# Optimization experiments

Measured on AMD Instinct MI355X. Metric: run time of the kernel, lower is better.

Reference implementation:

```python
import jax, jax.numpy as jnp
import numpy as np

B, N, M, K = 1, 200000, 100000, 16
C_IN, C_OUT, GFL, HEADS = 64, 128, 32, 8
C4 = C_OUT // 4          # 32, unary1 bottleneck width
C_MID = 16               # weightnet output channels


def _lin(key, fan_in, fan_out):
    return jax.random.normal(key, (fan_in, fan_out), jnp.float32) / np.sqrt(fan_in)


def setup_inputs() -> dict:
    key = jax.random.key(0)
    ks = jax.random.split(key, 20)
    return {
        'dense_xyz': jax.random.normal(ks[0], (B, N, 3), jnp.float32),
        'dense_feats': jax.random.normal(ks[1], (B, N, C_IN), jnp.float32),
        'dense_xyz_norm': jax.random.normal(ks[2], (B, N, 3), jnp.float32),
        'sparse_xyz': jax.random.normal(ks[3], (B, M, 3), jnp.float32),
        'sparse_xyz_norm': jax.random.normal(ks[4], (B, M, 3), jnp.float32),
        'vi_features': jax.random.normal(ks[5], (B, M, K, 12), jnp.float32),
        'nei_inds': jax.random.randint(ks[6], (B, M, K), 0, N),
        # unary1: in -> out/4 (Linear + BN(eval,init) + LeakyReLU(0.1))
        'w_unary1': _lin(ks[7], C_IN, C4), 'b_unary1': jnp.zeros((C4,), jnp.float32),
        # guidance_unary: out/4 -> GFL, no relu
        'w_gu': _lin(ks[8], C4, GFL), 'b_gu': jnp.zeros((GFL,), jnp.float32),
        # mlp_conv: 12 -> GFL (positional encoding on VI features)
        'w_pe': _lin(ks[9], 12, GFL), 'b_pe': jnp.zeros((GFL,), jnp.float32),
        # MultiHeadGuidance (subtraction): 2*GFL -> 8 -> HEADS
        'w_g1': _lin(ks[10], 2 * GFL, 8), 'b_g1': jnp.zeros((8,), jnp.float32),
        'w_g2': _lin(ks[11], 8, HEADS), 'b_g2': jnp.zeros((HEADS,), jnp.float32),
        # WeightNet: 12 -> 8 -> 8 -> 16, relu after each
        'w_wn1': _lin(ks[12], 12, 8), 'b_wn1': jnp.zeros((8,), jnp.float32),
        'w_wn2': _lin(ks[13], 8, 8), 'b_wn2': jnp.zeros((8,), jnp.float32),
        'w_wn3': _lin(ks[14], 8, C_MID), 'b_wn3': jnp.zeros((C_MID,), jnp.float32),
        # linear: out/4 * C_MID -> out/2
        'w_lin': _lin(ks[15], C4 * C_MID, C_OUT // 2), 'b_lin': jnp.zeros((C_OUT // 2,), jnp.float32),
        # unary2: out/2 -> out, no relu
        'w_u2': _lin(ks[16], C_OUT // 2, C_OUT), 'b_u2': jnp.zeros((C_OUT,), jnp.float32),
        # unary_shortcut: in -> out, no relu
        'w_sc': _lin(ks[17], C_IN, C_OUT), 'b_sc': jnp.zeros((C_OUT,), jnp.float32),
    }


def _gather(points, idx):
    # points: [B, N, C], idx: [B, M, K] int -> [B, M, K, C]
    return jax.vmap(lambda p, i: p[i])(points, idx)


def reference(dense_xyz, dense_feats, dense_xyz_norm, sparse_xyz, sparse_xyz_norm,
              vi_features, nei_inds,
              w_unary1, b_unary1, w_gu, b_gu, w_pe, b_pe,
              w_g1, b_g1, w_g2, b_g2,
              w_wn1, b_wn1, w_wn2, b_wn2, w_wn3, b_wn3,
              w_lin, b_lin, w_u2, b_u2, w_sc, b_sc):
    b, m, k = nei_inds.shape
    # unary1 (Linear+BN@init folds to Linear, LeakyReLU 0.1)
    feats_x = jax.nn.leaky_relu(dense_feats @ w_unary1 + b_unary1, 0.1)  # [B,N,C4]
    # USE_VI=True with precomputed vi_features -> weightNetInput = vi_features
    weightnet_input = vi_features                                        # [B,M,K,12]
    feat_pe = jax.nn.relu(weightnet_input @ w_pe + b_pe)                 # [B,M,K,GFL]
    guidance_x = feats_x @ w_gu + b_gu                                   # [B,N,GFL] (no_relu)
    gathered_g = _gather(guidance_x, nei_inds)                           # [B,M,K,GFL]
    g_feat = jnp.concatenate([gathered_g, feat_pe], axis=-1)             # [B,M,K,2*GFL]
    # subtraction guidance: query - max-pooled key over neighborhood
    scores = g_feat - jnp.max(g_feat, axis=2, keepdims=True)
    scores = jax.nn.relu(scores @ w_g1 + b_g1)
    scores = jax.nn.sigmoid(scores @ w_g2 + b_g2)                        # [B,M,K,H]
    gathered_feat = _gather(feats_x, nei_inds)                           # [B,M,K,C4]
    nf = gathered_feat.reshape(b, m, k, HEADS, C4 // HEADS) * scores[..., None]
    nf = nf.reshape(b, m, k, C4)
    # WeightNet on VI features
    w = jax.nn.relu(weightnet_input @ w_wn1 + b_wn1)
    w = jax.nn.relu(w @ w_wn2 + b_wn2)
    w = jax.nn.relu(w @ w_wn3 + b_wn3)                                   # [B,M,K,C_MID]
    # weighted neighbor aggregation: feat^T @ weights per point
    agg = jnp.einsum('bmkc,bmkw->bmcw', nf, w).reshape(b, m, C4 * C_MID)
    out = jax.nn.relu(agg @ w_lin + b_lin)                               # [B,M,out/2]
    out = out @ w_u2 + b_u2                                              # unary2, no relu
    # strided shortcut: max-pool dense feats over neighborhood, then unary
    sparse_feats = jnp.max(_gather(dense_feats, nei_inds), axis=2)       # [B,M,C_IN]
    shortcut = sparse_feats @ w_sc + b_sc
    return jax.nn.leaky_relu(out + shortcut, 0.1)                        # [B,M,C_OUT]
```

## Files before the change

### kernel.cpp

```cpp
#include <hip/hip_runtime.h>
#include <math.h>

typedef __attribute__((ext_vector_type(8))) __bf16 bf16x8;
typedef __attribute__((ext_vector_type(4))) __bf16 bf16x4;
typedef __attribute__((ext_vector_type(4))) float f32x4;

__device__ __forceinline__ float rowmax16(float x) {
    int xi = __builtin_bit_cast(int, x);
    float y;
    y = __builtin_bit_cast(float, __builtin_amdgcn_update_dpp(0, xi, 0x128, 0xf, 0xf, true));
    x = fmaxf(x, y); xi = __builtin_bit_cast(int, x);
    y = __builtin_bit_cast(float, __builtin_amdgcn_update_dpp(0, xi, 0x124, 0xf, 0xf, true));
    x = fmaxf(x, y); xi = __builtin_bit_cast(int, x);
    y = __builtin_bit_cast(float, __builtin_amdgcn_update_dpp(0, xi, 0x122, 0xf, 0xf, true));
    x = fmaxf(x, y); xi = __builtin_bit_cast(int, x);
    y = __builtin_bit_cast(float, __builtin_amdgcn_update_dpp(0, xi, 0x121, 0xf, 0xf, true));
    x = fmaxf(x, y);
    return x;
}

__global__ void prep_kernel(const float* __restrict__ wlin,
                            const float* __restrict__ wu2,
                            const float* __restrict__ wsc,
                            const float* __restrict__ w1,
                            const float* __restrict__ wg,
                            __bf16* __restrict__ wlinT,
                            __bf16* __restrict__ wu2T,
                            __bf16* __restrict__ wscT,
                            __bf16* __restrict__ w1Th,
                            __bf16* __restrict__ w1Tl,
                            __bf16* __restrict__ wgT)
{
    const int B0 = 64 * 512;
    const int B1 = B0 + 128 * 64;
    const int B2 = B1 + 128 * 64;
    const int B3 = B2 + 32 * 64;
    const int B4 = B3 + 32 * 32;
    int i = blockIdx.x * 256 + threadIdx.x;
    if (i < B0) {
        int l = i >> 9, k = i & 511;
        wlinT[i] = (__bf16)wlin[k * 64 + l];
    } else if (i < B1) {
        int j = i - B0; int co = j >> 6, kk = j & 63;
        wu2T[j] = (__bf16)wu2[kk * 128 + co];
    } else if (i < B2) {
        int j = i - B1; int co = j >> 6, kk = j & 63;
        wscT[j] = (__bf16)wsc[kk * 128 + co];
    } else if (i < B3) {
        int j = i - B2; int c = j >> 6, k = j & 63;
        float v = w1[k * 32 + c];
        __bf16 h = (__bf16)v;
        w1Th[j] = h;
        w1Tl[j] = (__bf16)(v - (float)h);
    } else if (i < B4) {
        int j = i - B3; int c = j >> 5, k = j & 31;
        wgT[j] = (__bf16)wg[k * 32 + c];
    }
}

__global__ __launch_bounds__(256) void feats_kernel(
    const float* __restrict__ df,
    const __bf16* __restrict__ w1Th, const __bf16* __restrict__ w1Tl,
    const float* __restrict__ b1,
    const __bf16* __restrict__ wgT, const float* __restrict__ bg,
    __bf16* __restrict__ fxb, __bf16* __restrict__ gxb,
    __bf16* __restrict__ dfb, int N)
{
    __shared__ __bf16 sFx[4][16][40];
    int t = threadIdx.x;
    int wv = t >> 6, ln = t & 63;
    int row = ln & 15, quad = ln >> 4;
    long n0 = (long)blockIdx.x * 64 + wv * 16;
    long n = n0 + row;
    bool ok = n < (long)N;

    const float4* dp = (const float4*)(df + (ok ? n * 64 : 0));
    float4 f00 = dp[quad * 2 + 0], f01 = dp[quad * 2 + 1];
    float4 f10 = dp[8 + quad * 2 + 0], f11 = dp[8 + quad * 2 + 1];
    float s0[8] = {f00.x, f00.y, f00.z, f00.w, f01.x, f01.y, f01.z, f01.w};
    float s1[8] = {f10.x, f10.y, f10.z, f10.w, f11.x, f11.y, f11.z, f11.w};
    bf16x8 aH0, aL0, aH1, aL1;
#pragma unroll
    for (int e = 0; e < 8; e++) {
        __bf16 h = (__bf16)s0[e]; aH0[e] = h; aL0[e] = (__bf16)(s0[e] - (float)h);
        __bf16 g = (__bf16)s1[e]; aH1[e] = g; aL1[e] = (__bf16)(s1[e] - (float)g);
    }
    if (ok) {
        *(bf16x8*)(dfb + n * 64 + quad * 8) = aH0;
        *(bf16x8*)(dfb + n * 64 + 32 + quad * 8) = aH1;
    }

    const __bf16* bh = w1Th + (row * 64 + quad * 8);
    const __bf16* bl = w1Tl + (row * 64 + quad * 8);
    f32x4 acc0 = {0.f, 0.f, 0.f, 0.f}, acc1 = {0.f, 0.f, 0.f, 0.f};
    {
        bf16x8 bH00 = *(const bf16x8*)(bh);
        bf16x8 bH01 = *(const bf16x8*)(bh + 32);
        bf16x8 bH10 = *(const bf16x8*)(bh + 16 * 64);
        bf16x8 bH11 = *(const bf16x8*)(bh + 16 * 64 + 32);
        bf16x8 bL00 = *(const bf16x8*)(bl);
        bf16x8 bL01 = *(const bf16x8*)(bl + 32);
        bf16x8 bL10 = *(const bf16x8*)(bl + 16 * 64);
        bf16x8 bL11 = *(const bf16x8*)(bl + 16 * 64 + 32);
        acc0 = __builtin_amdgcn_mfma_f32_16x16x32_bf16(aH0, bH00, acc0, 0, 0, 0);
        acc0 = __builtin_amdgcn_mfma_f32_16x16x32_bf16(aH1, bH01, acc0, 0, 0, 0);
        acc0 = __builtin_amdgcn_mfma_f32_16x16x32_bf16(aL0, bH00, acc0, 0, 0, 0);
        acc0 = __builtin_amdgcn_mfma_f32_16x16x32_bf16(aL1, bH01, acc0, 0, 0, 0);
        acc0 = __builtin_amdgcn_mfma_f32_16x16x32_bf16(aH0, bL00, acc0, 0, 0, 0);
        acc0 = __builtin_amdgcn_mfma_f32_16x16x32_bf16(aH1, bL01, acc0, 0, 0, 0);
        acc1 = __builtin_amdgcn_mfma_f32_16x16x32_bf16(aH0, bH10, acc1, 0, 0, 0);
        acc1 = __builtin_amdgcn_mfma_f32_16x16x32_bf16(aH1, bH11, acc1, 0, 0, 0);
        acc1 = __builtin_amdgcn_mfma_f32_16x16x32_bf16(aL0, bH10, acc1, 0, 0, 0);
        acc1 = __builtin_amdgcn_mfma_f32_16x16x32_bf16(aL1, bH11, acc1, 0, 0, 0);
        acc1 = __builtin_amdgcn_mfma_f32_16x16x32_bf16(aH0, bL10, acc1, 0, 0, 0);
        acc1 = __builtin_amdgcn_mfma_f32_16x16x32_bf16(aH1, bL11, acc1, 0, 0, 0);
    }
    {
        float bb0 = b1[row], bb1 = b1[16 + row];
#pragma unroll
        for (int r = 0; r < 4; r++) {
            float x0 = acc0[r] + bb0; x0 = x0 > 0.f ? x0 : 0.1f * x0;
            float x1 = acc1[r] + bb1; x1 = x1 > 0.f ? x1 : 0.1f * x1;
            sFx[wv][quad * 4 + r][row] = (__bf16)x0;
            sFx[wv][quad * 4 + r][16 + row] = (__bf16)x1;
        }
    }
    __builtin_amdgcn_s_waitcnt(0);

    f32x4 g0 = {0.f, 0.f, 0.f, 0.f}, g1 = {0.f, 0.f, 0.f, 0.f};
    {
        bf16x8 a2 = *(const bf16x8*)(&sFx[wv][row][quad * 8]);
        bf16x8 b20 = *(const bf16x8*)(wgT + row * 32 + quad * 8);
        bf16x8 b21 = *(const bf16x8*)(wgT + (16 + row) * 32 + quad * 8);
        g0 = __builtin_amdgcn_mfma_f32_16x16x32_bf16(a2, b20, g0, 0, 0, 0);
        g1 = __builtin_amdgcn_mfma_f32_16x16x32_bf16(a2, b21, g1, 0, 0, 0);
    }
    {
        int r16 = ln >> 2, seg = ln & 3;
        bf16x8 vfx = *(const bf16x8*)(&sFx[wv][r16][seg * 8]);
        long nn = n0 + r16;
        if (nn < (long)N) *(bf16x8*)(fxb + nn * 32 + seg * 8) = vfx;
    }
    {
        float bb0 = bg[row], bb1 = bg[16 + row];
#pragma unroll
        for (int r = 0; r < 4; r++) {
            sFx[wv][quad * 4 + r][row] = (__bf16)(g0[r] + bb0);
            sFx[wv][quad * 4 + r][16 + row] = (__bf16)(g1[r] + bb1);
        }
    }
    __builtin_amdgcn_s_waitcnt(0);
    {
        int r16 = ln >> 2, seg = ln & 3;
        bf16x8 vg = *(const bf16x8*)(&sFx[wv][r16][seg * 8]);
        long nn = n0 + r16;
        if (nn < (long)N) *(bf16x8*)(gxb + nn * 32 + seg * 8) = vg;
    }
}

struct SmemU {
    union {
        struct { __bf16 nfF[16 * 512]; __bf16 w3A[16 * 256]; } a;
        __bf16 aggB[16][520];
    };
};

__global__ __launch_bounds__(256, 5) void pcf_kernel(
    const float* __restrict__ vi, const int* __restrict__ nei,
    const __bf16* __restrict__ fxb, const __bf16* __restrict__ gxb,
    const __bf16* __restrict__ dfb,
    const float* __restrict__ wpe, const float* __restrict__ bpe,
    const float* __restrict__ wg1, const float* __restrict__ bg1,
    const float* __restrict__ wg2, const float* __restrict__ bg2,
    const float* __restrict__ wn1, const float* __restrict__ bn1,
    const float* __restrict__ wn2, const float* __restrict__ bn2,
    const float* __restrict__ wn3, const float* __restrict__ bn3,
    const __bf16* __restrict__ wlinT, const float* __restrict__ blin,
    const __bf16* __restrict__ wu2T, const float* __restrict__ bu2,
    const __bf16* __restrict__ wscT, const float* __restrict__ bsc,
    float* __restrict__ out, int M)
{
    __shared__ SmemU U;
    __shared__ __bf16 sO[16][72];
    __shared__ __bf16 sS[16][72];
    __shared__ int sInd[16][16];

    int t = threadIdx.x;
    int p = t >> 4, q = t & 15;
    long mbase = (long)blockIdx.x * 16;
    long m = mbase + p;
    bool okm = m < (long)M;
    int ind = okm ? nei[m * 16 + q] : 0;
    sInd[p][q] = ind;

    float v[12];
    {
        const float4* v4 = (const float4*)(vi + (okm ? (m * 16 + q) * 12 : 0));
        float4 a = v4[0], b = v4[1], cc = v4[2];
        v[0] = a.x; v[1] = a.y; v[2] = a.z; v[3] = a.w;
        v[4] = b.x; v[5] = b.y; v[6] = b.z; v[7] = b.w;
        v[8] = cc.x; v[9] = cc.y; v[10] = cc.z; v[11] = cc.w;
    }
    {
        float wa[8], wb[8];
#pragma unroll
        for (int j = 0; j < 8; j++) {
            float a = bn1[j];
#pragma unroll
            for (int i = 0; i < 12; i++) a += v[i] * wn1[i * 8 + j];
            wa[j] = fmaxf(a, 0.f);
        }
#pragma unroll
        for (int j = 0; j < 8; j++) {
            float a = bn2[j];
#pragma unroll
            for (int i = 0; i < 8; i++) a += wa[i] * wn2[i * 8 + j];
            wb[j] = fmaxf(a, 0.f);
        }
        int swz = (p & 3) << 4;
        int kb = (q >> 3) * 128 + (q & 7);
#pragma unroll
        for (int j = 0; j < 16; j++) {
            float a = bn3[j];
#pragma unroll
            for (int i = 0; i < 8; i++) a += wb[i] * wn3[i * 16 + j];
            U.a.w3A[p * 256 + ((kb + j * 8) ^ swz)] = (__bf16)fmaxf(a, 0.f);
        }
    }
    float pe[32];
#pragma unroll
    for (int c = 0; c < 32; c++) {
        float a = bpe[c];
#pragma unroll
        for (int i = 0; i < 12; i++) a += v[i] * wpe[i * 32 + c];
        pe[c] = fmaxf(a, 0.f);
    }
    float gd[32];
    {
        const bf16x8* g8 = (const bf16x8*)(gxb + (long)ind * 32);
#pragma unroll
        for (int c8 = 0; c8 < 4; c8++) {
            bf16x8 g = g8[c8];
#pragma unroll
            for (int e = 0; e < 8; e++) gd[c8 * 8 + e] = (float)g[e];
        }
    }
    float s1[8];
#pragma unroll
    for (int j = 0; j < 8; j++) s1[j] = bg1[j];
#pragma unroll
    for (int i = 0; i < 64; i++) {
        float gi = (i < 32) ? gd[i] : pe[i - 32];
        float sub = gi - rowmax16(gi);
#pragma unroll
        for (int j = 0; j < 8; j++) s1[j] += sub * wg1[i * 8 + j];
    }
#pragma unroll
    for (int j = 0; j < 8; j++) s1[j] = fmaxf(s1[j], 0.f);
    float s2[8];
#pragma unroll
    for (int j = 0; j < 8; j++) {
        float a = bg2[j];
#pragma unroll
        for (int i = 0; i < 8; i++) a += s1[i] * wg2[i * 8 + j];
        s2[j] = 1.f / (1.f + __expf(-a));
    }
    {
        const bf16x8* f8 = (const bf16x8*)(fxb + (long)ind * 32);
        int swz = (p & 3) << 4;
#pragma unroll
        for (int g = 0; g < 4; g++) {
            bf16x8 f = f8[g];
            float sA = s2[2 * g], sB = s2[2 * g + 1];
#pragma unroll
            for (int e = 0; e < 8; e++) {
                int c = g * 8 + e;
                float val = (float)f[e] * (e < 4 ? sA : sB);
                U.a.nfF[p * 512 + ((((c >> 4) * 256) + (c & 15) * 16 + q) ^ swz)] = (__bf16)val;
            }
        }
    }
    {
        float4 mx = make_float4(-1e30f, -1e30f, -1e30f, -1e30f);
#pragma unroll
        for (int kk = 0; kk < 16; kk++) {
            int ik = sInd[p][kk];
            bf16x4 d = *(const bf16x4*)(dfb + (long)ik * 64 + q * 4);
            mx.x = fmaxf(mx.x, (float)d[0]); mx.y = fmaxf(mx.y, (float)d[1]);
            mx.z = fmaxf(mx.z, (float)d[2]); mx.w = fmaxf(mx.w, (float)d[3]);
        }
        bf16x4 pk;
        pk[0] = (__bf16)mx.x; pk[1] = (__bf16)mx.y; pk[2] = (__bf16)mx.z; pk[3] = (__bf16)mx.w;
        *(bf16x4*)(&sS[p][q * 4]) = pk;
    }

    {
        int wv2 = t >> 6, ln2 = t & 63;
        int col = ln2 & 15, quad = ln2 >> 4;
        bf16x8 z8 = {};
        bf16x4 dpk[4][2];
#pragma unroll
        for (int pp = 0; pp < 4; pp++) {
            int p2 = wv2 * 4 + pp;
            int swz = (p2 & 3) << 4;
            bf16x8 afr = z8, bf0 = z8, bf1 = z8;
            if (quad < 2) {
                afr = *(const bf16x8*)(&U.a.w3A[p2 * 256 + ((quad * 128 + col * 8) ^ swz)]);
                bf0 = *(const bf16x8*)(&U.a.nfF[p2 * 512 + ((col * 16 + quad * 8) ^ swz)]);
                bf1 = *(const bf16x8*)(&U.a.nfF[p2 * 512 + ((256 + col * 16 + quad * 8) ^ swz)]);
            }
            f32x4 ac0 = {0.f, 0.f, 0.f, 0.f}, ac1 = {0.f, 0.f, 0.f, 0.f};
            ac0 = __builtin_amdgcn_mfma_f32_16x16x32_bf16(afr, bf0, ac0, 0, 0, 0);
            ac1 = __builtin_amdgcn_mfma_f32_16x16x32_bf16(afr, bf1, ac1, 0, 0, 0);
#pragma unroll
            for (int r = 0; r < 4; r++) {
                dpk[pp][0][r] = (__bf16)ac0[r];
                dpk[pp][1][r] = (__bf16)ac1[r];
            }
        }
        __syncthreads();
#pragma unroll
        for (int pp = 0; pp < 4; pp++) {
            int p2 = wv2 * 4 + pp;
            *(bf16x4*)(&U.aggB[p2][col * 16 + quad * 4]) = dpk[pp][0];
            *(bf16x4*)(&U.aggB[p2][(16 + col) * 16 + quad * 4]) = dpk[pp][1];
        }
    }
    __syncthreads();

    {
        int wv = t >> 6, ln = t & 63;
        int n = ln & 15, quad = ln >> 4;
        const __bf16* Bp = wlinT + ((wv * 16 + n) * 512 + quad * 8);
        f32x4 acc = {0.f, 0.f, 0.f, 0.f};
#pragma unroll
        for (int kk = 0; kk < 16; kk++) {
            bf16x8 a = *(const bf16x8*)(&U.aggB[n][kk * 32 + quad * 8]);
            bf16x8 b = *(const bf16x8*)(Bp + kk * 32);
            acc = __builtin_amdgcn_mfma_f32_16x16x32_bf16(a, b, acc, 0, 0, 0);
        }
        int col = wv * 16 + n;
        float bl = blin[col];
#pragma unroll
        for (int r = 0; r < 4; r++) {
            int row = quad * 4 + r;
            sO[row][col] = (__bf16)fmaxf(acc[r] + bl, 0.f);
        }
    }
    __syncthreads();

    {
        int wv = t >> 6, ln = t & 63;
        int n = ln & 15, quad = ln >> 4;
        bf16x8 aO0 = *(const bf16x8*)(&sO[n][quad * 8]);
        bf16x8 aO1 = *(const bf16x8*)(&sO[n][32 + quad * 8]);
        bf16x8 aS0 = *(const bf16x8*)(&sS[n][quad * 8]);
        bf16x8 aS1 = *(const bf16x8*)(&sS[n][32 + quad * 8]);
#pragma unroll
        for (int tt = 0; tt < 2; tt++) {
            int T = wv * 2 + tt;
            int col = T * 16 + n;
            const __bf16* B1 = wu2T + (col * 64 + quad * 8);
            const __bf16* B2 = wscT + (col * 64 + quad * 8);
            f32x4 acc = {0.f, 0.f, 0.f, 0.f};
            acc = __builtin_amdgcn_mfma_f32_16x16x32_bf16(aO0, *(const bf16x8*)(B1), acc, 0, 0, 0);
            acc = __builtin_amdgcn_mfma_f32_16x16x32_bf16(aO1, *(const bf16x8*)(B1 + 32), acc, 0, 0, 0);
            acc = __builtin_amdgcn_mfma_f32_16x16x32_bf16(aS0, *(const bf16x8*)(B2), acc, 0, 0, 0);
            acc = __builtin_amdgcn_mfma_f32_16x16x32_bf16(aS1, *(const bf16x8*)(B2 + 32), acc, 0, 0, 0);
            float bb = bu2[col] + bsc[col];
#pragma unroll
            for (int r = 0; r < 4; r++) {
                long mm = mbase + quad * 4 + r;
                if (mm < (long)M) {
                    float x = acc[r] + bb;
                    out[mm * 128 + col] = x > 0.f ? x : 0.1f * x;
                }
            }
        }
    }
}

extern "C" void kernel_launch(void* const* d_in, const int* in_sizes, int n_in,
                              void* d_out, int out_size, void* d_ws, size_t ws_size,
                              hipStream_t stream)
{
    const float* dense_feats = (const float*)d_in[1];
    const float* vi    = (const float*)d_in[5];
    const int*   nei   = (const int*)d_in[6];
    const float* w_u1  = (const float*)d_in[7];
    const float* b_u1  = (const float*)d_in[8];
    const float* w_gu  = (const float*)d_in[9];
    const float* b_gu  = (const float*)d_in[10];
    const float* w_pe  = (const float*)d_in[11];
    const float* b_pe  = (const float*)d_in[12];
    const float* w_g1  = (const float*)d_in[13];
    const float* b_g1  = (const float*)d_in[14];
    const float* w_g2  = (const float*)d_in[15];
    const float* b_g2  = (const float*)d_in[16];
    const float* w_wn1 = (const float*)d_in[17];
    const float* b_wn1 = (const float*)d_in[18];
    const float* w_wn2 = (const float*)d_in[19];
    const float* b_wn2 = (const float*)d_in[20];
    const float* w_wn3 = (const float*)d_in[21];
    const float* b_wn3 = (const float*)d_in[22];
    const float* w_lin = (const float*)d_in[23];
    const float* b_lin = (const float*)d_in[24];
    const float* w_u2  = (const float*)d_in[25];
    const float* b_u2  = (const float*)d_in[26];
    const float* w_sc  = (const float*)d_in[27];
    const float* b_sc  = (const float*)d_in[28];

    int N = in_sizes[1] / 64;
    int M = in_sizes[6] / 16;

    __bf16* fxb  = (__bf16*)d_ws;
    __bf16* gxb  = fxb + (size_t)N * 32;
    __bf16* dfb  = gxb + (size_t)N * 32;
    __bf16* wlinT = dfb + (size_t)N * 64;
    __bf16* wu2T  = wlinT + 64 * 512;
    __bf16* wscT  = wu2T + 128 * 64;
    __bf16* w1Th  = wscT + 128 * 64;
    __bf16* w1Tl  = w1Th + 32 * 64;
    __bf16* wgT   = w1Tl + 32 * 64;

    const int prep_items = 64 * 512 + 2 * 128 * 64 + 2 * 32 * 64 + 32 * 32;
    prep_kernel<<<(prep_items + 255) / 256, 256, 0, stream>>>(
        w_lin, w_u2, w_sc, w_u1, w_gu, wlinT, wu2T, wscT, w1Th, w1Tl, wgT);

    feats_kernel<<<(N + 63) / 64, 256, 0, stream>>>(
        dense_feats, w1Th, w1Tl, b_u1, wgT, b_gu, fxb, gxb, dfb, N);

    pcf_kernel<<<(M + 15) / 16, 256, 0, stream>>>(
        vi, nei, fxb, gxb, dfb,
        w_pe, b_pe, w_g1, b_g1, w_g2, b_g2,
        w_wn1, b_wn1, w_wn2, b_wn2, w_wn3, b_wn3,
        wlinT, b_lin, wu2T, b_u2, wscT, b_sc,
        (float*)d_out, M);
}
```

Before: 378.8 us.

## Use packed fp16 dot2 for small per-neighbor MLPs and guidance max

The per-neighbor scalar MLPs (weightnet, positional encoding, guidance layers) now run with fp16 inputs packed two per register and v_dot2 f32 accumulation. Their weights are pre-packed into half2 pairs in the prep kernel. The guidance features are stored as fp16 instead of bf16, so the subtract-max reduction can use packed half2 DPP max. This roughly halves the FMA and DPP instruction count in the ALU-heavy front part of pcf_kernel, at the cost of fp16 range and precision on the activations.

Measured after the change: 369.7 us. 2.4% less time.

```diff
diff --git a/kernel.cpp b/kernel.cpp
--- a/kernel.cpp
+++ b/kernel.cpp
@@ -4,19 +4,42 @@
 typedef __attribute__((ext_vector_type(8))) __bf16 bf16x8;
 typedef __attribute__((ext_vector_type(4))) __bf16 bf16x4;
 typedef __attribute__((ext_vector_type(4))) float f32x4;
-
-__device__ __forceinline__ float rowmax16(float x) {
+typedef __attribute__((ext_vector_type(8))) unsigned short ushort8;
+typedef __attribute__((ext_vector_type(2))) _Float16 h2;
+
+__device__ __forceinline__ float fdot2(h2 a, h2 b, float c) {
+#if __has_builtin(__builtin_amdgcn_fdot2)
+    return __builtin_amdgcn_fdot2(a, b, c, false);
+#else
+    return c + (float)a[0] * (float)b[0] + (float)a[1] * (float)b[1];
+#endif
+}
+
+__device__ __forceinline__ h2 h2max(h2 a, h2 b) {
+#if __has_builtin(__builtin_elementwise_max)
+    return __builtin_elementwise_max(a, b);
+#else
+    h2 r; r[0] = a[0] > b[0] ? a[0] : b[0]; r[1] = a[1] > b[1] ? a[1] : b[1]; return r;
+#endif
+}
+
+__device__ __forceinline__ h2 rowmax16h(h2 x) {
     int xi = __builtin_bit_cast(int, x);
-    float y;
-    y = __builtin_bit_cast(float, __builtin_amdgcn_update_dpp(0, xi, 0x128, 0xf, 0xf, true));
-    x = fmaxf(x, y); xi = __builtin_bit_cast(int, x);
-    y = __builtin_bit_cast(float, __builtin_amdgcn_update_dpp(0, xi, 0x124, 0xf, 0xf, true));
-    x = fmaxf(x, y); xi = __builtin_bit_cast(int, x);
-    y = __builtin_bit_cast(float, __builtin_amdgcn_update_dpp(0, xi, 0x122, 0xf, 0xf, true));
-    x = fmaxf(x, y); xi = __builtin_bit_cast(int, x);
-    y = __builtin_bit_cast(float, __builtin_amdgcn_update_dpp(0, xi, 0x121, 0xf, 0xf, true));
-    x = fmaxf(x, y);
+    int y;
+    y = __builtin_amdgcn_update_dpp(0, xi, 0x128, 0xf, 0xf, true);
+    x = h2max(x, __builtin_bit_cast(h2, y)); xi = __builtin_bit_cast(int, x);
+    y = __builtin_amdgcn_update_dpp(0, xi, 0x124, 0xf, 0xf, true);
+    x = h2max(x, __builtin_bit_cast(h2, y)); xi = __builtin_bit_cast(int, x);
+    y = __builtin_amdgcn_update_dpp(0, xi, 0x122, 0xf, 0xf, true);
+    x = h2max(x, __builtin_bit_cast(h2, y)); xi = __builtin_bit_cast(int, x);
+    y = __builtin_amdgcn_update_dpp(0, xi, 0x121, 0xf, 0xf, true);
+    x = h2max(x, __builtin_bit_cast(h2, y));
     return x;
+}
+
+__device__ __forceinline__ unsigned int packh2(float a, float b) {
+    h2 v = { (_Float16)a, (_Float16)b };
+    return __builtin_bit_cast(unsigned int, v);
 }
 
 __global__ void prep_kernel(const float* __restrict__ wlin,
@@ -24,18 +47,31 @@
                             const float* __restrict__ wsc,
                             const float* __restrict__ w1,
                             const float* __restrict__ wg,
+                            const float* __restrict__ wg1,
+                            const float* __restrict__ wpe,
+                            const float* __restrict__ wn1,
+                            const float* __restrict__ wn2,
+                            const float* __restrict__ wn3,
+                            const float* __restrict__ wg2,
                             __bf16* __restrict__ wlinT,
                             __bf16* __restrict__ wu2T,
                             __bf16* __restrict__ wscT,
                             __bf16* __restrict__ w1Th,
                             __bf16* __restrict__ w1Tl,
-                            __bf16* __restrict__ wgT)
+                            __bf16* __restrict__ wgT,
+                            unsigned int* __restrict__ pk)
 {
     const int B0 = 64 * 512;
     const int B1 = B0 + 128 * 64;
     const int B2 = B1 + 128 * 64;
     const int B3 = B2 + 32 * 64;
     const int B4 = B3 + 32 * 32;
+    const int B5 = B4 + 256;
+    const int B6 = B5 + 192;
+    const int B7 = B6 + 48;
+    const int B8 = B7 + 32;
+    const int B9 = B8 + 64;
+    const int B10 = B9 + 32;
     int i = blockIdx.x * 256 + threadIdx.x;
     if (i < B0) {
         int l = i >> 9, k = i & 511;
@@ -55,6 +91,24 @@
     } else if (i < B4) {
         int j = i - B3; int c = j >> 5, k = j & 31;
         wgT[j] = (__bf16)wg[k * 32 + c];
+    } else if (i < B5) {
+        int j2 = i - B4; int t = j2 >> 3, j = j2 & 7;
+        pk[j2] = packh2(wg1[(2 * t) * 8 + j], wg1[(2 * t + 1) * 8 + j]);
+    } else if (i < B6) {
+        int j2 = i - B5; int t = j2 >> 5, c = j2 & 31;
+        pk[256 + j2] = packh2(wpe[(2 * t) * 32 + c], wpe[(2 * t + 1) * 32 + c]);
+    } else if (i < B7) {
+        int j2 = i - B6; int t = j2 >> 3, j = j2 & 7;
+        pk[448 + j2] = packh2(wn1[(2 * t) * 8 + j], wn1[(2 * t + 1) * 8 + j]);
+    } else if (i < B8) {
+        int j2 = i - B7; int t = j2 >> 3, j = j2 & 7;
+        pk[496 + j2] = packh2(wn2[(2 * t) * 8 + j], wn2[(2 * t + 1) * 8 + j]);
+    } else if (i < B9) {
+        int j2 = i - B8; int t = j2 >> 4, j = j2 & 15;
+        pk[528 + j2] = packh2(wn3[(2 * t) * 16 + j], wn3[(2 * t + 1) * 16 + j]);
+    } else if (i < B10) {
+        int j2 = i - B9; int t = j2 >> 3, j = j2 & 7;
+        pk[592 + j2] = packh2(wg2[(2 * t) * 8 + j], wg2[(2 * t + 1) * 8 + j]);
     }
 }
 
@@ -63,10 +117,10 @@
     const __bf16* __restrict__ w1Th, const __bf16* __restrict__ w1Tl,
     const float* __restrict__ b1,
     const __bf16* __restrict__ wgT, const float* __restrict__ bg,
-    __bf16* __restrict__ fxb, __bf16* __restrict__ gxb,
+    __bf16* __restrict__ fxb, unsigned short* __restrict__ gxh,
     __bf16* __restrict__ dfb, int N)
 {
-    __shared__ __bf16 sFx[4][16][40];
+    __shared__ unsigned short sFx[4][16][40];
     int t = threadIdx.x;
     int wv = t >> 6, ln = t & 63;
     int row = ln & 15, quad = ln >> 4;
@@ -121,15 +175,15 @@
         for (int r = 0; r < 4; r++) {
             float x0 = acc0[r] + bb0; x0 = x0 > 0.f ? x0 : 0.1f * x0;
             float x1 = acc1[r] + bb1; x1 = x1 > 0.f ? x1 : 0.1f * x1;
-            sFx[wv][quad * 4 + r][row] = (__bf16)x0;
-            sFx[wv][quad * 4 + r][16 + row] = (__bf16)x1;
+            sFx[wv][quad * 4 + r][row] = __builtin_bit_cast(unsigned short, (__bf16)x0);
+            sFx[wv][quad * 4 + r][16 + row] = __builtin_bit_cast(unsigned short, (__bf16)x1);
         }
     }
     __builtin_amdgcn_s_waitcnt(0);
 
     f32x4 g0 = {0.f, 0.f, 0.f, 0.f}, g1 = {0.f, 0.f, 0.f, 0.f};
     {
-        bf16x8 a2 = *(const bf16x8*)(&sFx[wv][row][quad * 8]);
+        bf16x8 a2 = __builtin_bit_cast(bf16x8, *(const ushort8*)(&sFx[wv][row][quad * 8]));
         bf16x8 b20 = *(const bf16x8*)(wgT + row * 32 + quad * 8);
         bf16x8 b21 = *(const bf16x8*)(wgT + (16 + row) * 32 + quad * 8);
         g0 = __builtin_amdgcn_mfma_f32_16x16x32_bf16(a2, b20, g0, 0, 0, 0);
@@ -137,24 +191,24 @@
     }
     {
         int r16 = ln >> 2, seg = ln & 3;
-        bf16x8 vfx = *(const bf16x8*)(&sFx[wv][r16][seg * 8]);
+        ushort8 vfx = *(const ushort8*)(&sFx[wv][r16][seg * 8]);
         long nn = n0 + r16;
-        if (nn < (long)N) *(bf16x8*)(fxb + nn * 32 + seg * 8) = vfx;
+        if (nn < (long)N) *(ushort8*)((unsigned short*)fxb + nn * 32 + seg * 8) = vfx;
     }
     {
         float bb0 = bg[row], bb1 = bg[16 + row];
 #pragma unroll
         for (int r = 0; r < 4; r++) {
-            sFx[wv][quad * 4 + r][row] = (__bf16)(g0[r] + bb0);
-            sFx[wv][quad * 4 + r][16 + row] = (__bf16)(g1[r] + bb1);
+            sFx[wv][quad * 4 + r][row] = __builtin_bit_cast(unsigned short, (_Float16)(g0[r] + bb0));
+            sFx[wv][quad * 4 + r][16 + row] = __builtin_bit_cast(unsigned short, (_Float16)(g1[r] + bb1));
         }
     }
     __builtin_amdgcn_s_waitcnt(0);
     {
         int r16 = ln >> 2, seg = ln & 3;
-        bf16x8 vg = *(const bf16x8*)(&sFx[wv][r16][seg * 8]);
+        ushort8 vg = *(const ushort8*)(&sFx[wv][r16][seg * 8]);
         long nn = n0 + r16;
-        if (nn < (long)N) *(bf16x8*)(gxb + nn * 32 + seg * 8) = vg;
+        if (nn < (long)N) *(ushort8*)(gxh + nn * 32 + seg * 8) = vg;
     }
 }
 
@@ -167,14 +221,13 @@
 
 __global__ __launch_bounds__(256, 5) void pcf_kernel(
     const float* __restrict__ vi, const int* __restrict__ nei,
-    const __bf16* __restrict__ fxb, const __bf16* __restrict__ gxb,
+    const __bf16* __restrict__ fxb, const unsigned short* __restrict__ gxh,
     const __bf16* __restrict__ dfb,
-    const float* __restrict__ wpe, const float* __restrict__ bpe,
-    const float* __restrict__ wg1, const float* __restrict__ bg1,
-    const float* __restrict__ wg2, const float* __restrict__ bg2,
-    const float* __restrict__ wn1, const float* __restrict__ bn1,
-    const float* __restrict__ wn2, const float* __restrict__ bn2,
-    const float* __restrict__ wn3, const float* __restrict__ bn3,
+    const unsigned int* __restrict__ pk,
+    const float* __restrict__ bpe,
+    const float* __restrict__ bg1, const float* __restrict__ bg2,
+    const float* __restrict__ bn1, const float* __restrict__ bn2,
+    const float* __restrict__ bn3,
     const __bf16* __restrict__ wlinT, const float* __restrict__ blin,
     const __bf16* __restrict__ wu2T, const float* __restrict__ bu2,
     const __bf16* __restrict__ wscT, const float* __restrict__ bsc,
@@ -185,6 +238,13 @@
     __shared__ __bf16 sS[16][72];
     __shared__ int sInd[16][16];
 
+    const unsigned int* wg1P = pk;
+    const unsigned int* wpeP = pk + 256;
+    const unsigned int* wn1P = pk + 448;
+    const unsigned int* wn2P = pk + 496;
+    const unsigned int* wn3P = pk + 528;
+    const unsigned int* wg2P = pk + 592;
+
     int t = threadIdx.x;
     int p = t >> 4, q = t & 15;
     long mbase = (long)blockIdx.x * 16;
@@ -193,76 +253,96 @@
     int ind = okm ? nei[m * 16 + q] : 0;
     sInd[p][q] = ind;
 
-    float v[12];
+    h2 vh[6];
     {
         const float4* v4 = (const float4*)(vi + (okm ? (m * 16 + q) * 12 : 0));
         float4 a = v4[0], b = v4[1], cc = v4[2];
-        v[0] = a.x; v[1] = a.y; v[2] = a.z; v[3] = a.w;
-        v[4] = b.x; v[5] = b.y; v[6] = b.z; v[7] = b.w;
-        v[8] = cc.x; v[9] = cc.y; v[10] = cc.z; v[11] = cc.w;
-    }
-    {
-        float wa[8], wb[8];
+        vh[0] = (h2){(_Float16)a.x, (_Float16)a.y};
+        vh[1] = (h2){(_Float16)a.z, (_Float16)a.w};
+        vh[2] = (h2){(_Float16)b.x, (_Float16)b.y};
+        vh[3] = (h2){(_Float16)b.z, (_Float16)b.w};
+        vh[4] = (h2){(_Float16)cc.x, (_Float16)cc.y};
+        vh[5] = (h2){(_Float16)cc.z, (_Float16)cc.w};
+    }
+    {
+        float wa[8];
 #pragma unroll
         for (int j = 0; j < 8; j++) {
             float a = bn1[j];
 #pragma unroll
-            for (int i = 0; i < 12; i++) a += v[i] * wn1[i * 8 + j];
+            for (int tt2 = 0; tt2 < 6; tt2++)
+                a = fdot2(vh[tt2], __builtin_bit_cast(h2, wn1P[tt2 * 8 + j]), a);
             wa[j] = fmaxf(a, 0.f);
         }
+        h2 wah[4];
+#pragma unroll
+        for (int tt2 = 0; tt2 < 4; tt2++)
+            wah[tt2] = (h2){(_Float16)wa[2 * tt2], (_Float16)wa[2 * tt2 + 1]};
+        float wb[8];
 #pragma unroll
         for (int j = 0; j < 8; j++) {
             float a = bn2[j];
 #pragma unroll
-            for (int i = 0; i < 8; i++) a += wa[i] * wn2[i * 8 + j];
+            for (int tt2 = 0; tt2 < 4; tt2++)
+                a = fdot2(wah[tt2], __builtin_bit_cast(h2, wn2P[tt2 * 8 + j]), a);
             wb[j] = fmaxf(a, 0.f);
         }
+        h2 wbh[4];
+#pragma unroll
+        for (int tt2 = 0; tt2 < 4; tt2++)
+            wbh[tt2] = (h2){(_Float16)wb[2 * tt2], (_Float16)wb[2 * tt2 + 1]};
         int swz = (p & 3) << 4;
         int kb = (q >> 3) * 128 + (q & 7);
 #pragma unroll
         for (int j = 0; j < 16; j++) {
             float a = bn3[j];
 #pragma unroll
-            for (int i = 0; i < 8; i++) a += wb[i] * wn3[i * 16 + j];
+            for (int tt2 = 0; tt2 < 4; tt2++)
+                a = fdot2(wbh[tt2], __builtin_bit_cast(h2, wn3P[tt2 * 16 + j]), a);
             U.a.w3A[p * 256 + ((kb + j * 8) ^ swz)] = (__bf16)fmaxf(a, 0.f);
         }
     }
-    float pe[32];
-#pragma unroll
-    for (int c = 0; c < 32; c++) {
-        float a = bpe[c];
-#pragma unroll
-        for (int i = 0; i < 12; i++) a += v[i] * wpe[i * 32 + c];
-        pe[c] = fmaxf(a, 0.f);
-    }
-    float gd[32];
-    {
-        const bf16x8* g8 = (const bf16x8*)(gxb + (long)ind * 32);
-#pragma unroll
-        for (int c8 = 0; c8 < 4; c8++) {
-            bf16x8 g = g8[c8];
-#pragma unroll
-            for (int e = 0; e < 8; e++) gd[c8 * 8 + e] = (float)g[e];
-        }
+    h2 peh[16];
+#pragma unroll
+    for (int c2 = 0; c2 < 16; c2++) {
+        float a0 = bpe[2 * c2], a1 = bpe[2 * c2 + 1];
+#pragma unroll
+        for (int tt2 = 0; tt2 < 6; tt2++) {
+            a0 = fdot2(vh[tt2], __builtin_bit_cast(h2, wpeP[tt2 * 32 + 2 * c2]), a0);
+            a1 = fdot2(vh[tt2], __builtin_bit_cast(h2, wpeP[tt2 * 32 + 2 * c2 + 1]), a1);
+        }
+        peh[c2] = (h2){(_Float16)fmaxf(a0, 0.f), (_Float16)fmaxf(a1, 0.f)};
+    }
+    h2 gdh[16];
+    {
+        const unsigned int* gu = (const unsigned int*)(gxh + (long)ind * 32);
+#pragma unroll
+        for (int tt2 = 0; tt2 < 16; tt2++)
+            gdh[tt2] = __builtin_bit_cast(h2, gu[tt2]);
     }
     float s1[8];
 #pragma unroll
     for (int j = 0; j < 8; j++) s1[j] = bg1[j];
 #pragma unroll
-    for (int i = 0; i < 64; i++) {
-        float gi = (i < 32) ? gd[i] : pe[i - 32];
-        float sub = gi - rowmax16(gi);
-#pragma unroll
-        for (int j = 0; j < 8; j++) s1[j] += sub * wg1[i * 8 + j];
-    }
-#pragma unroll
-    for (int j = 0; j < 8; j++) s1[j] = fmaxf(s1[j], 0.f);
+    for (int tt2 = 0; tt2 < 32; tt2++) {
+        h2 g2 = (tt2 < 16) ? gdh[tt2] : peh[tt2 - 16];
+        h2 m2 = rowmax16h(g2);
+        h2 sub = g2 - m2;
+#pragma unroll
+        for (int j = 0; j < 8; j++)
+            s1[j] = fdot2(sub, __builtin_bit_cast(h2, wg1P[tt2 * 8 + j]), s1[j]);
+    }
+    h2 s1h[4];
+#pragma unroll
+    for (int tt2 = 0; tt2 < 4; tt2++)
+        s1h[tt2] = (h2){(_Float16)fmaxf(s1[2 * tt2], 0.f), (_Float16)fmaxf(s1[2 * tt2 + 1], 0.f)};
     float s2[8];
 #pragma unroll
     for (int j = 0; j < 8; j++) {
         float a = bg2[j];
 #pragma unroll
-        for (int i = 0; i < 8; i++) a += s1[i] * wg2[i * 8 + j];
+        for (int tt2 = 0; tt2 < 4; tt2++)
+            a = fdot2(s1h[tt2], __builtin_bit_cast(h2, wg2P[tt2 * 8 + j]), a);
         s2[j] = 1.f / (1.f + __expf(-a));
     }
     {
@@ -289,9 +369,9 @@
             mx.x = fmaxf(mx.x, (float)d[0]); mx.y = fmaxf(mx.y, (float)d[1]);
             mx.z = fmaxf(mx.z, (float)d[2]); mx.w = fmaxf(mx.w, (float)d[3]);
         }
-        bf16x4 pk;
-        pk[0] = (__bf16)mx.x; pk[1] = (__bf16)mx.y; pk[2] = (__bf16)mx.z; pk[3] = (__bf16)mx.w;
-        *(bf16x4*)(&sS[p][q * 4]) = pk;
+        bf16x4 pkk;
+        pkk[0] = (__bf16)mx.x; pkk[1] = (__bf16)mx.y; pkk[2] = (__bf16)mx.z; pkk[3] = (__bf16)mx.w;
+        *(bf16x4*)(&sS[p][q * 4]) = pkk;
     }
 
     {
@@ -414,26 +494,27 @@
     int M = in_sizes[6] / 16;
 
     __bf16* fxb  = (__bf16*)d_ws;
-    __bf16* gxb  = fxb + (size_t)N * 32;
-    __bf16* dfb  = gxb + (size_t)N * 32;
+    unsigned short* gxh = (unsigned short*)(fxb + (size_t)N * 32);
+    __bf16* dfb  = (__bf16*)(gxh + (size_t)N * 32);
     __bf16* wlinT = dfb + (size_t)N * 64;
     __bf16* wu2T  = wlinT + 64 * 512;
     __bf16* wscT  = wu2T + 128 * 64;
     __bf16* w1Th  = wscT + 128 * 64;
     __bf16* w1Tl  = w1Th + 32 * 64;
     __bf16* wgT   = w1Tl + 32 * 64;
-
-    const int prep_items = 64 * 512 + 2 * 128 * 64 + 2 * 32 * 64 + 32 * 32;
+    unsigned int* pk = (unsigned int*)(wgT + 32 * 32);
+
+    const int prep_items = 64 * 512 + 2 * 128 * 64 + 2 * 32 * 64 + 32 * 32 + 624;
     prep_kernel<<<(prep_items + 255) / 256, 256, 0, stream>>>(
-        w_lin, w_u2, w_sc, w_u1, w_gu, wlinT, wu2T, wscT, w1Th, w1Tl, wgT);
+        w_lin, w_u2, w_sc, w_u1, w_gu, w_g1, w_pe, w_wn1, w_wn2, w_wn3, w_g2,
+        wlinT, wu2T, wscT, w1Th, w1Tl, wgT, pk);
 
     feats_kernel<<<(N + 63) / 64, 256, 0, stream>>>(
-        dense_feats, w1Th, w1Tl, b_u1, wgT, b_gu, fxb, gxb, dfb, N);
+        dense_feats, w1Th, w1Tl, b_u1, wgT, b_gu, fxb, gxh, dfb, N);
 
     pcf_kernel<<<(M + 15) / 16, 256, 0, stream>>>(
-        vi, nei, fxb, gxb, dfb,
-        w_pe, b_pe, w_g1, b_g1, w_g2, b_g2,
-        w_wn1, b_wn1, w_wn2, b_wn2, w_wn3, b_wn3,
+        vi, nei, fxb, gxh, dfb, pk,
+        b_pe, b_g1, b_g2, b_wn1, b_wn2, b_wn3,
         wlinT, b_lin, wu2T, b_u2, wscT, b_sc,
         (float*)d_out, M);
 }
```
